# Performance work log

Measured on AMD Instinct MI355X. Metric: run time of the kernel, lower is better.

Reference implementation:

```python
import jax, jax.numpy as jnp
import numpy as np

B, P, T, V, N, D = 16, 96, 128, 64, 16, 128


def setup_inputs() -> dict:
    key = jax.random.key(0)
    ks = jax.random.split(key, 9)
    s = 0.05  # weight scale for stability
    return {
        "queries": jax.random.normal(ks[0], (B, P, V, D), jnp.float32),
        "keys": jax.random.normal(ks[1], (B, T, V, D), jnp.float32),
        "var_ccc": jax.random.randint(ks[2], (B, V, N), 0, V),
        "Wq": jax.random.normal(ks[3], (D, D), jnp.float32) * s,
        "bq": jnp.zeros((D,), jnp.float32),
        "Wkv": jax.random.normal(ks[4], (D, D), jnp.float32) * s,
        "bkv": jnp.zeros((D,), jnp.float32),
        "Wout": jax.random.normal(ks[5], (D, D), jnp.float32) * s,
        "bout": jnp.zeros((D,), jnp.float32),
    }


def reference(queries, keys, var_ccc, Wq, bq, Wkv, bkv, Wout, bout):
    b, p, v, d = queries.shape
    scale = d ** -0.5
    # projections (nn.Linear: x @ W.T + b)
    q = queries @ Wq.T + bq                      # [B,P,V,D]
    k = keys @ Wkv.T + bkv                       # [B,T,V,D]
    k_last = k[:, -p:]                           # [B,P,V,D]
    # irregular gather of neighbor keys per (batch, variable)
    idx = var_ccc.reshape(b, -1)                 # [B, V*N]
    kc = jax.vmap(lambda kb, ib: kb[:, ib])(k_last, idx)  # [B,P,V*N,D]
    kc = kc.reshape(b, p, v, -1, d)              # [B,P,V,N,D] (keys == values)
    # tiny 1xN attention per (b,p,v)
    scores = jnp.einsum('bpvd,bpvnd->bpvn', q, kc) * scale
    attn = jax.nn.softmax(scores, axis=-1)       # dropout is identity in eval
    out = jnp.einsum('bpvn,bpvnd->bpvd', attn, kc)  # [B,P,V,D]
    res = jnp.concatenate([k[:, :-p], out], axis=1)  # [B,T,V,D]
    return res @ Wout.T + bout
```

## Files before the change

### kernel.cpp

```cpp
#include <hip/hip_runtime.h>

#define BB 16
#define PP 96
#define TT 128
#define VV 64
#define NN 16
#define DD 128
#define BPP (BB * PP)
#define NPASS (BB * 32)
#define SB 136
#define ST 72
#define SSF 68
#define SCALE 0.08838834764831845f
#define SLICE 4352

typedef __bf16 bf16x8 __attribute__((ext_vector_type(8)));
typedef __bf16 bf16x4 __attribute__((ext_vector_type(4)));
typedef float  floatx4 __attribute__((ext_vector_type(4)));
typedef unsigned int uint32x4 __attribute__((ext_vector_type(4)));

#define MFMA16(a, b, c) __builtin_amdgcn_mfma_f32_16x16x32_bf16(a, b, c, 0, 0, 0)

__device__ __forceinline__ bf16x8 cvt8(float4 a, float4 b) {
    return bf16x8{(__bf16)a.x, (__bf16)a.y, (__bf16)a.z, (__bf16)a.w,
                  (__bf16)b.x, (__bf16)b.y, (__bf16)b.z, (__bf16)b.w};
}

__device__ __forceinline__ void loadA_g(const float* Xs, int lm, int lq, bf16x8 af[4]) {
    const float4* p = (const float4*)(Xs + lm * DD + lq * 8);
#pragma unroll
    for (int ks = 0; ks < 4; ++ks) af[ks] = cvt8(p[8 * ks], p[8 * ks + 1]);
}

__device__ __forceinline__ void loadA_l(const __bf16* As, int sa, int lm, int lq,
                                        bf16x8* af, int kblocks) {
#pragma unroll
    for (int ks = 0; ks < 4; ++ks) {
        if (ks >= kblocks) break;
        af[ks] = *(const bf16x8*)(As + lm * sa + lq * 8 + 32 * ks);
    }
}

__device__ __forceinline__ void mmB(const bf16x8* af, const __bf16* B, int sb,
                                    int lm, int lq, floatx4* acc, int nblocks, int kblocks) {
#pragma unroll
    for (int nb = 0; nb < 8; ++nb) {
        if (nb >= nblocks) break;
        acc[nb] = floatx4{0.f, 0.f, 0.f, 0.f};
#pragma unroll
        for (int ks = 0; ks < 4; ++ks) {
            if (ks >= kblocks) break;
            bf16x8 bf = *(const bf16x8*)(B + (nb * 16 + lm) * sb + lq * 8 + 32 * ks);
            acc[nb] = MFMA16(af[ks], bf, acc[nb]);
        }
    }
}

__global__ void prep(const float* __restrict__ Wq, const float* __restrict__ Wkv,
                     const float* __restrict__ Wout, const float* __restrict__ bq,
                     const float* __restrict__ bkv, const float* __restrict__ bout,
                     __bf16* __restrict__ Wb, float* __restrict__ bcomb,
                     float* __restrict__ bqk) {
    int i = blockIdx.x, j = threadIdx.x;
    float m1[4] = {0.f, 0.f, 0.f, 0.f}, wc[4] = {0.f, 0.f, 0.f, 0.f};
    for (int k = 0; k < DD; k += 4) {
#pragma unroll
        for (int u = 0; u < 4; ++u) {
            m1[u] += Wq[(k + u) * DD + j] * Wkv[(k + u) * DD + i];
            wc[u] += Wout[i * DD + k + u] * Wkv[(k + u) * DD + j];
        }
    }
    Wb[i * DD + j]         = (__bf16)((m1[0] + m1[1]) + (m1[2] + m1[3]));
    Wb[16384 + i * DD + j] = (__bf16)((wc[0] + wc[1]) + (wc[2] + wc[3]));
    if (i == 0) {
        float bs[4] = {bout[j], 0.f, 0.f, 0.f}, bk[4] = {0.f, 0.f, 0.f, 0.f};
        for (int k = 0; k < DD; k += 4) {
#pragma unroll
            for (int u = 0; u < 4; ++u) {
                bs[u] += Wout[j * DD + k + u] * bkv[k + u];
                bk[u] += bq[k + u] * Wkv[(k + u) * DD + j];
            }
        }
        bcomb[j] = (bs[0] + bs[1]) + (bs[2] + bs[3]);
        bqk[j]   = (bk[0] + bk[1]) + (bk[2] + bk[3]);
    }
}

__global__ __launch_bounds__(256, 4) void fused(
    const float* __restrict__ queries, const float* __restrict__ keys,
    const int* __restrict__ ccc, const __bf16* __restrict__ Wb,
    const float* __restrict__ bqk, const float* __restrict__ bcomb,
    float* __restrict__ out) {
    __shared__ __align__(16) char lds[35840];
    __bf16* R1    = (__bf16*)lds;
    __bf16* smKCT = (__bf16*)(lds + 17408);
    float*  smS   = (float*)lds;

    int bl = blockIdx.x, t = threadIdx.x;
    int w = t >> 6, L = t & 63, lm = L & 15, lq = L >> 4;

    bf16x8 af[4];
    floatx4 acc[8];

    if (bl >= BPP) {
        int pb = bl - BPP;
        int b = pb >> 5, wi = pb & 31;
        const float* Xs = keys + ((long)b * TT * VV + wi * 64 + w * 16) * DD;
        float* Yg = out + ((long)b * TT * VV + wi * 64) * DD;
        loadA_g(Xs, lm, lq, af);
        mmB(af, Wb + 16384, DD, lm, lq, acc, 8, 4);
#pragma unroll
        for (int nb = 0; nb < 8; ++nb) {
            float bv = bcomb[nb * 16 + lm];
#pragma unroll
            for (int r = 0; r < 4; ++r)
                Yg[(long)(w * 16 + lq * 4 + r) * DD + nb * 16 + lm] = acc[nb][r] + bv;
        }
        return;
    }

    int b = bl / PP, p = bl % PP;
    const float* Qg = queries + ((long)(b * PP + p) * VV) * DD;
    const float* Kg = keys + ((long)(b * TT + 32 + p) * VV) * DD;
    float* Yg = out + ((long)(b * TT + 32 + p) * VV) * DD;

    float4 kr[8];
    {
        const float4* kp = (const float4*)(Kg + (w * 16 + lm) * DD + lq * 8);
#pragma unroll
        for (int ks = 0; ks < 4; ++ks) {
            kr[2 * ks] = kp[8 * ks]; kr[2 * ks + 1] = kp[8 * ks + 1];
        }
    }

#pragma unroll
    for (int ks = 0; ks < 4; ++ks) af[ks] = cvt8(kr[2 * ks], kr[2 * ks + 1]);
    mmB(af, Wb + 16384, DD, lm, lq, acc, 8, 4);

    float4 qr[8];
    {
        const float4* qp = (const float4*)(Qg + (w * 16 + lm) * DD + lq * 8);
#pragma unroll
        for (int ks = 0; ks < 4; ++ks) {
            qr[2 * ks] = qp[8 * ks]; qr[2 * ks + 1] = qp[8 * ks + 1];
        }
    }

#pragma unroll
    for (int nb = 0; nb < 8; ++nb) {
        bf16x4 tp;
#pragma unroll
        for (int r = 0; r < 4; ++r) tp[r] = (__bf16)acc[nb][r];
        *(bf16x4*)(smKCT + (nb * 16 + lm) * ST + w * 16 + lq * 4) = tp;
    }

#pragma unroll
    for (int ks = 0; ks < 4; ++ks) af[ks] = cvt8(qr[2 * ks], qr[2 * ks + 1]);
    mmB(af, Wb, DD, lm, lq, acc, 8, 4);
#pragma unroll
    for (int nb = 0; nb < 8; ++nb) {
        float bv = bqk[nb * 16 + lm];
#pragma unroll
        for (int r = 0; r < 4; ++r)
            R1[(w * 16 + lq * 4 + r) * SB + nb * 16 + lm] = (__bf16)(acc[nb][r] + bv);
    }

    int se[NN];
    {
        const int4* cp = (const int4*)(ccc + ((long)b * VV + w * 16 + lm) * NN);
#pragma unroll
        for (int i = 0; i < 4; ++i) {
            int4 c4 = cp[i];
            se[4 * i] = c4.x; se[4 * i + 1] = c4.y;
            se[4 * i + 2] = c4.z; se[4 * i + 3] = c4.w;
        }
    }

    loadA_l(R1 + w * 16 * SB, SB, lm, lq, af, 4);
#pragma unroll
    for (int nb = 0; nb < 4; ++nb) {
        float4 kb[8];
        const float4* kp = (const float4*)(Kg + (nb * 16 + lm) * DD + lq * 8);
#pragma unroll
        for (int ks = 0; ks < 4; ++ks) {
            kb[2 * ks] = kp[8 * ks]; kb[2 * ks + 1] = kp[8 * ks + 1];
        }
        acc[nb] = floatx4{0.f, 0.f, 0.f, 0.f};
#pragma unroll
        for (int ks = 0; ks < 4; ++ks)
            acc[nb] = MFMA16(af[ks], cvt8(kb[2 * ks], kb[2 * ks + 1]), acc[nb]);
    }
#pragma unroll
    for (int nb = 0; nb < 4; ++nb)
#pragma unroll
        for (int r = 0; r < 4; ++r)
            smS[(w * 16 + lq * 4 + r) * SSF + nb * 16 + lm] = acc[nb][r];

    __bf16* smAsl = (__bf16*)(lds + w * SLICE);
    {
        int g = lq;
        float sg[NN];
        const float* Srow = smS + (w * 16 + lm) * SSF;
#pragma unroll
        for (int n = 0; n < NN; ++n) sg[n] = Srow[se[n]];
        __builtin_amdgcn_sched_barrier(0);
        {
            uint32x4 z{0u, 0u, 0u, 0u};
            char* zb = (char*)smAsl + (L >> 2) * (ST * 2) + (L & 3) * 32;
            *(uint32x4*)zb = z;
            *(uint32x4*)(zb + 16) = z;
        }
        float mx = -1e30f;
#pragma unroll
        for (int n = 0; n < NN; ++n) { sg[n] *= SCALE; mx = fmaxf(mx, sg[n]); }
        float sum = 0.f;
#pragma unroll
        for (int n = 0; n < NN; ++n) { sg[n] = __expf(sg[n] - mx); sum += sg[n]; }
        float inv = 1.f / sum;
#pragma unroll
        for (int j = 0; j < 4; ++j) {
            int u = se[g * 4 + j];
            float tot = 0.f;
#pragma unroll
            for (int n = 0; n < NN; ++n) tot += (se[n] == u) ? sg[n] : 0.f;
            smAsl[lm * ST + u] = (__bf16)(tot * inv);
        }
    }
    __syncthreads();

    loadA_l(smAsl, ST, lm, lq, af, 2);
    mmB(af, smKCT, ST, lm, lq, acc, 8, 2);
#pragma unroll
    for (int nb = 0; nb < 8; ++nb) {
        float bv = bcomb[nb * 16 + lm];
#pragma unroll
        for (int r = 0; r < 4; ++r)
            Yg[(long)(w * 16 + lq * 4 + r) * DD + nb * 16 + lm] = acc[nb][r] + bv;
    }
}

extern "C" void kernel_launch(void* const* d_in, const int* in_sizes, int n_in,
                              void* d_out, int out_size, void* d_ws, size_t ws_size,
                              hipStream_t stream) {
    const float* queries = (const float*)d_in[0];
    const float* keys    = (const float*)d_in[1];
    const int*   ccc     = (const int*)d_in[2];
    const float* Wq      = (const float*)d_in[3];
    const float* bq      = (const float*)d_in[4];
    const float* Wkv     = (const float*)d_in[5];
    const float* bkv     = (const float*)d_in[6];
    const float* Wout    = (const float*)d_in[7];
    const float* bout    = (const float*)d_in[8];
    float* out = (float*)d_out;

    __bf16* Wb    = (__bf16*)d_ws;
    float*  bcomb = (float*)((char*)d_ws + 65536);
    float*  bqk   = (float*)((char*)d_ws + 66048);

    prep<<<dim3(128), dim3(128), 0, stream>>>(Wq, Wkv, Wout, bq, bkv, bout, Wb, bcomb, bqk);

    fused<<<dim3(BPP + NPASS), dim3(256), 0, stream>>>(
        queries, keys, ccc, Wb, bqk, bcomb, out);
}
```

Baseline: 244.5 us.

## Reassociate score product to project keys by Wkv^T Wq instead of queries

Instead of projecting each query row through Wq^T Wkv and then multiplying by the raw keys from global memory, the kernel now projects the key tile through the transposed combined matrix into LDS and multiplies the raw queries against it. The bq-derived bias term becomes a per-key scalar computed with one extra MFMA and added during the score gather. This removes the second global read and fp32-to-bf16 conversion of the key tile in the score stage, reusing the already-loaded keys. In exchange LDS grows to about 52 KB, occupancy bounds drop from 4 to 3 blocks, and a barrier moves earlier in the block.

```diff
diff --git a/kernel.cpp b/kernel.cpp
--- a/kernel.cpp
+++ b/kernel.cpp
@@ -59,41 +59,45 @@
 __global__ void prep(const float* __restrict__ Wq, const float* __restrict__ Wkv,
                      const float* __restrict__ Wout, const float* __restrict__ bq,
                      const float* __restrict__ bkv, const float* __restrict__ bout,
-                     __bf16* __restrict__ Wb, float* __restrict__ bcomb,
-                     float* __restrict__ bqk) {
+                     __bf16* __restrict__ Wb, float* __restrict__ bcomb) {
     int i = blockIdx.x, j = threadIdx.x;
-    float m1[4] = {0.f, 0.f, 0.f, 0.f}, wc[4] = {0.f, 0.f, 0.f, 0.f};
+    float m2[4] = {0.f, 0.f, 0.f, 0.f}, wc[4] = {0.f, 0.f, 0.f, 0.f};
     for (int k = 0; k < DD; k += 4) {
 #pragma unroll
         for (int u = 0; u < 4; ++u) {
-            m1[u] += Wq[(k + u) * DD + j] * Wkv[(k + u) * DD + i];
+            m2[u] += Wq[(k + u) * DD + i] * Wkv[(k + u) * DD + j];
             wc[u] += Wout[i * DD + k + u] * Wkv[(k + u) * DD + j];
         }
     }
-    Wb[i * DD + j]         = (__bf16)((m1[0] + m1[1]) + (m1[2] + m1[3]));
+    Wb[i * DD + j]         = (__bf16)((m2[0] + m2[1]) + (m2[2] + m2[3]));
     Wb[16384 + i * DD + j] = (__bf16)((wc[0] + wc[1]) + (wc[2] + wc[3]));
+    if (i < 16) {
+        float bk[4] = {0.f, 0.f, 0.f, 0.f};
+        for (int k = 0; k < DD; k += 4) {
+#pragma unroll
+            for (int u = 0; u < 4; ++u) bk[u] += bq[k + u] * Wkv[(k + u) * DD + j];
+        }
+        Wb[32768 + i * DD + j] = (__bf16)((bk[0] + bk[1]) + (bk[2] + bk[3]));
+    }
     if (i == 0) {
-        float bs[4] = {bout[j], 0.f, 0.f, 0.f}, bk[4] = {0.f, 0.f, 0.f, 0.f};
+        float bs[4] = {bout[j], 0.f, 0.f, 0.f};
         for (int k = 0; k < DD; k += 4) {
 #pragma unroll
-            for (int u = 0; u < 4; ++u) {
-                bs[u] += Wout[j * DD + k + u] * bkv[k + u];
-                bk[u] += bq[k + u] * Wkv[(k + u) * DD + j];
-            }
+            for (int u = 0; u < 4; ++u) bs[u] += Wout[j * DD + k + u] * bkv[k + u];
         }
         bcomb[j] = (bs[0] + bs[1]) + (bs[2] + bs[3]);
-        bqk[j]   = (bk[0] + bk[1]) + (bk[2] + bk[3]);
-    }
-}
-
-__global__ __launch_bounds__(256, 4) void fused(
+    }
+}
+
+__global__ __launch_bounds__(256, 3) void fused(
     const float* __restrict__ queries, const float* __restrict__ keys,
     const int* __restrict__ ccc, const __bf16* __restrict__ Wb,
-    const float* __restrict__ bqk, const float* __restrict__ bcomb,
-    float* __restrict__ out) {
-    __shared__ __align__(16) char lds[35840];
+    const float* __restrict__ bcomb, float* __restrict__ out) {
+    __shared__ __align__(16) char lds[53504];
     __bf16* R1    = (__bf16*)lds;
-    __bf16* smKCT = (__bf16*)(lds + 17408);
+    __bf16* smKM  = (__bf16*)(lds + 17408);
+    __bf16* smKCT = (__bf16*)(lds + 34816);
+    float*  smSB  = (float*)(lds + 53248);
     float*  smS   = (float*)lds;
 
     int bl = blockIdx.x, t = threadIdx.x;
@@ -154,15 +158,23 @@
         *(bf16x4*)(smKCT + (nb * 16 + lm) * ST + w * 16 + lq * 4) = tp;
     }
 
-#pragma unroll
-    for (int ks = 0; ks < 4; ++ks) af[ks] = cvt8(qr[2 * ks], qr[2 * ks + 1]);
     mmB(af, Wb, DD, lm, lq, acc, 8, 4);
-#pragma unroll
-    for (int nb = 0; nb < 8; ++nb) {
-        float bv = bqk[nb * 16 + lm];
+
+    floatx4 sbacc{0.f, 0.f, 0.f, 0.f};
+#pragma unroll
+    for (int ks = 0; ks < 4; ++ks) {
+        bf16x8 bf = *(const bf16x8*)(Wb + 32768 + lm * DD + lq * 8 + 32 * ks);
+        sbacc = MFMA16(af[ks], bf, sbacc);
+    }
+
+#pragma unroll
+    for (int nb = 0; nb < 8; ++nb)
 #pragma unroll
         for (int r = 0; r < 4; ++r)
-            R1[(w * 16 + lq * 4 + r) * SB + nb * 16 + lm] = (__bf16)(acc[nb][r] + bv);
+            smKM[(w * 16 + lq * 4 + r) * SB + nb * 16 + lm] = (__bf16)acc[nb][r];
+    if (lm == 0) {
+#pragma unroll
+        for (int r = 0; r < 4; ++r) smSB[w * 16 + lq * 4 + r] = sbacc[r];
     }
 
     int se[NN];
@@ -175,21 +187,11 @@
             se[4 * i + 2] = c4.z; se[4 * i + 3] = c4.w;
         }
     }
-
-    loadA_l(R1 + w * 16 * SB, SB, lm, lq, af, 4);
-#pragma unroll
-    for (int nb = 0; nb < 4; ++nb) {
-        float4 kb[8];
-        const float4* kp = (const float4*)(Kg + (nb * 16 + lm) * DD + lq * 8);
-#pragma unroll
-        for (int ks = 0; ks < 4; ++ks) {
-            kb[2 * ks] = kp[8 * ks]; kb[2 * ks + 1] = kp[8 * ks + 1];
-        }
-        acc[nb] = floatx4{0.f, 0.f, 0.f, 0.f};
-#pragma unroll
-        for (int ks = 0; ks < 4; ++ks)
-            acc[nb] = MFMA16(af[ks], cvt8(kb[2 * ks], kb[2 * ks + 1]), acc[nb]);
-    }
+    __syncthreads();
+
+#pragma unroll
+    for (int ks = 0; ks < 4; ++ks) af[ks] = cvt8(qr[2 * ks], qr[2 * ks + 1]);
+    mmB(af, smKM, SB, lm, lq, acc, 4, 4);
 #pragma unroll
     for (int nb = 0; nb < 4; ++nb)
 #pragma unroll
@@ -202,7 +204,7 @@
         float sg[NN];
         const float* Srow = smS + (w * 16 + lm) * SSF;
 #pragma unroll
-        for (int n = 0; n < NN; ++n) sg[n] = Srow[se[n]];
+        for (int n = 0; n < NN; ++n) sg[n] = Srow[se[n]] + smSB[se[n]];
         __builtin_amdgcn_sched_barrier(0);
         {
             uint32x4 z{0u, 0u, 0u, 0u};
@@ -226,7 +228,6 @@
             smAsl[lm * ST + u] = (__bf16)(tot * inv);
         }
     }
-    __syncthreads();
 
     loadA_l(smAsl, ST, lm, lq, af, 2);
     mmB(af, smKCT, ST, lm, lq, acc, 8, 2);
@@ -254,11 +255,10 @@
     float* out = (float*)d_out;
 
     __bf16* Wb    = (__bf16*)d_ws;
-    float*  bcomb = (float*)((char*)d_ws + 65536);
-    float*  bqk   = (float*)((char*)d_ws + 66048);
-
-    prep<<<dim3(128), dim3(128), 0, stream>>>(Wq, Wkv, Wout, bq, bkv, bout, Wb, bcomb, bqk);
+    float*  bcomb = (float*)((char*)d_ws + 98304);
+
+    prep<<<dim3(128), dim3(128), 0, stream>>>(Wq, Wkv, Wout, bq, bkv, bout, Wb, bcomb);
 
     fused<<<dim3(BPP + NPASS), dim3(256), 0, stream>>>(
-        queries, keys, ccc, Wb, bqk, bcomb, out);
-}
+        queries, keys, ccc, Wb, bcomb, out);
+}
```

New measurement: 229.5 us. 1.07x faster.
